# Kernel tuning notes

Measured on AMD Instinct MI355X. Metric: run time of the kernel, lower is better.

Reference implementation:

```python
import jax, jax.numpy as jnp
import numpy as np

B, S, H = 4, 2048, 1024
NH = 16
HD = H // NH  # 64


def setup_inputs() -> dict:
    key = jax.random.key(0)
    ks = jax.random.split(key, 9)
    s = 1.0 / np.sqrt(H)
    inp = {
        "x": jax.random.normal(ks[0], (B, S, H), dtype=jnp.float32),
        "wq": jax.random.normal(ks[1], (H, H), dtype=jnp.float32) * s,
        "bq": jnp.zeros((H,), dtype=jnp.float32),
        "wk": jax.random.normal(ks[2], (H, H), dtype=jnp.float32) * s,
        "bk": jnp.zeros((H,), dtype=jnp.float32),
        "wv": jax.random.normal(ks[3], (H, H), dtype=jnp.float32) * s,
        "bv": jnp.zeros((H,), dtype=jnp.float32),
        "wo": jax.random.normal(ks[4], (H, H), dtype=jnp.float32) * s,
        "bo": jnp.zeros((H,), dtype=jnp.float32),
    }
    return inp


def _split_heads(t):
    # [B,S,H] -> [B,NH,S,HD]
    return t.reshape(B, S, NH, HD).transpose(0, 2, 1, 3)


def reference(x, wq, bq, wk, bk, wv, bv, wo, bo):
    # Linear layers (torch Linear: x @ W^T + b; weights here stored as [in,out])
    q = _split_heads(x @ wq + bq)
    k = _split_heads(x @ wk + bk)
    v = _split_heads(x @ wv + bv)
    scale = 1.0 / jnp.sqrt(jnp.asarray(HD, dtype=x.dtype))
    scores = jnp.einsum("bhqd,bhkd->bhqk", q, k) * scale  # [B,NH,S,S]
    attn = jax.nn.softmax(scores, axis=-1)
    ctx = jnp.einsum("bhqk,bhkd->bhqd", attn, v)  # [B,NH,S,HD]
    ctx = ctx.transpose(0, 2, 1, 3).reshape(B, S, H)
    return ctx @ wo + bo
```

## Files before the change

kernel.cpp:

```cpp
#include <hip/hip_runtime.h>
#include <hip/hip_bf16.h>
#include <math.h>

typedef __bf16 bf16;
typedef __attribute__((ext_vector_type(4))) __bf16 bf16x4;
typedef __attribute__((ext_vector_type(8))) __bf16 bf16x8;
typedef __attribute__((ext_vector_type(4))) float f32x4;

#define B_  4
#define S_  2048
#define H_  1024
#define NH_ 16
#define HD_ 64
#define M_  (B_ * S_)

#define LP 72

__device__ __forceinline__ f32x4 mfma16(bf16x8 a, bf16x8 b, f32x4 c) {
    return __builtin_amdgcn_mfma_f32_16x16x32_bf16(a, b, c, 0, 0, 0);
}

__device__ __forceinline__ void glds16(const bf16* g, bf16* l) {
    __builtin_amdgcn_global_load_lds(
        (const __attribute__((address_space(1))) void*)g,
        (__attribute__((address_space(3))) void*)l, 16, 0, 0);
}

__global__ __launch_bounds__(256) void cvt_bf16(const float* __restrict__ in,
                                                bf16* __restrict__ out) {
    const size_t i = ((size_t)blockIdx.x * 256 + threadIdx.x) * 8;
    float4 f0 = *(const float4*)&in[i];
    float4 f1 = *(const float4*)&in[i + 4];
    bf16x8 v;
    v[0] = (bf16)f0.x; v[1] = (bf16)f0.y; v[2] = (bf16)f0.z; v[3] = (bf16)f0.w;
    v[4] = (bf16)f1.x; v[5] = (bf16)f1.y; v[6] = (bf16)f1.z; v[7] = (bf16)f1.w;
    *(bf16x8*)&out[i] = v;
}

__global__ __launch_bounds__(256) void transpose_w(const float* __restrict__ in,
                                                   bf16* __restrict__ out) {
    __shared__ bf16 tile[64][65];
    const int t = threadIdx.x;
    const int bx = blockIdx.x * 64, by = blockIdx.y * 64;
#pragma unroll
    for (int i = 0; i < 16; ++i) {
        int idx = i * 256 + t;
        int r = idx >> 6, c = idx & 63;
        tile[r][c] = (bf16)in[(by + r) * 1024 + bx + c];
    }
    __syncthreads();
#pragma unroll
    for (int i = 0; i < 16; ++i) {
        int idx = i * 256 + t;
        int r = idx >> 6, c = idx & 63;
        out[(bx + r) * 1024 + by + c] = tile[c][r];
    }
}

template <typename TC0>
__global__ __launch_bounds__(256) void gemm_glds(const bf16* __restrict__ A,
                                                 const bf16* __restrict__ Bt,
                                                 const float* __restrict__ b0,
                                                 const float* __restrict__ b1,
                                                 const float* __restrict__ b2,
                                                 TC0* __restrict__ out0,
                                                 bf16* __restrict__ out1,
                                                 bf16* __restrict__ out2t,
                                                 float scale0) {
    __shared__ alignas(16) bf16 As[128 * 64];
    __shared__ alignas(16) bf16 Bs[128 * 64];
    const int t = threadIdx.x;
    const int m0 = blockIdx.x * 128;
    const int n0 = blockIdx.y * 128;
    const int lane = t & 63, w = t >> 6;
    const int quad = lane >> 4, l15 = lane & 15;
    const int wm = w >> 1, wn = w & 1;
    const int srow = lane >> 3;
    const int scol = (lane & 7) * 8;

    const bf16* Ab = A + (size_t)(m0 + srow) * 1024 + scol;
    const bf16* Bb = Bt + (size_t)(n0 + srow) * 1024 + scol;

    f32x4 acc[4][4];
#pragma unroll
    for (int i = 0; i < 4; ++i)
#pragma unroll
        for (int j = 0; j < 4; ++j) acc[i][j] = (f32x4){0.f, 0.f, 0.f, 0.f};

    for (int kt = 0; kt < 16; ++kt) {
#pragma unroll
        for (int i = 0; i < 4; ++i) {
            const int c = w * 4 + i;
            glds16(Ab + (size_t)c * 8 * 1024 + kt * 64, &As[c * 512]);
            glds16(Bb + (size_t)c * 8 * 1024 + kt * 64, &Bs[c * 512]);
        }
        __syncthreads();
#pragma unroll
        for (int ks = 0; ks < 2; ++ks) {
            bf16x8 a[4], b[4];
#pragma unroll
            for (int mi = 0; mi < 4; ++mi)
                a[mi] = *(const bf16x8*)&As[(wm * 64 + mi * 16 + l15) * 64 + ks * 32 + quad * 8];
#pragma unroll
            for (int ni = 0; ni < 4; ++ni)
                b[ni] = *(const bf16x8*)&Bs[(wn * 64 + ni * 16 + l15) * 64 + ks * 32 + quad * 8];
#pragma unroll
            for (int mi = 0; mi < 4; ++mi)
#pragma unroll
                for (int ni = 0; ni < 4; ++ni)
                    acc[mi][ni] = mfma16(a[mi], b[ni], acc[mi][ni]);
        }
        __syncthreads();
    }

    const int seg = n0 >> 10;
    const float* bias = (seg == 0) ? b0 : (seg == 1) ? b1 : b2;
#pragma unroll
    for (int ni = 0; ni < 4; ++ni) {
        const int coln = (n0 & 1023) + wn * 64 + ni * 16 + l15;
        const float bcol = bias[coln];
#pragma unroll
        for (int mi = 0; mi < 4; ++mi) {
            const int row0 = m0 + wm * 64 + mi * 16 + quad * 4;
            if (seg == 2) {
                bf16x4 v;
#pragma unroll
                for (int r = 0; r < 4; ++r) v[r] = (bf16)(acc[mi][ni][r] + bcol);
                *(bf16x4*)&out2t[(size_t)coln * M_ + row0] = v;
            } else if (seg == 1) {
#pragma unroll
                for (int r = 0; r < 4; ++r)
                    out1[(size_t)(row0 + r) * 1024 + coln] = (bf16)(acc[mi][ni][r] + bcol);
            } else {
#pragma unroll
                for (int r = 0; r < 4; ++r)
                    out0[(size_t)(row0 + r) * 1024 + coln] =
                        (TC0)((acc[mi][ni][r] + bcol) * scale0);
            }
        }
    }
}

__global__ __launch_bounds__(256, 4) void attn(const bf16* Q,
                                               const bf16* __restrict__ K,
                                               const bf16* __restrict__ Vt,
                                               bf16* O) {
    __shared__ alignas(16) bf16 smem[128 * LP];
    bf16* Ks = smem;
    bf16* Vs = smem + 64 * LP;

    const int t = threadIdx.x;
    const int lane = t & 63, w = t >> 6;
    const int quad = lane >> 4, l15 = lane & 15;
    const int bh = blockIdx.x;
    const int q0 = blockIdx.y * 128;
    const int b = bh >> 4, h = bh & 15;
    const bf16* qp  = Q + (size_t)b * S_ * H_ + h * HD_;
    const bf16* kp  = K + (size_t)b * S_ * H_ + h * HD_;
    const bf16* vtp = Vt + (size_t)(h * HD_) * M_ + b * S_;

    const int r0 = t >> 3, r1 = 32 + (t >> 3);
    const int kc = (t & 7) * 8;
    const int s0 = ((((r0 >> 4) & 2) | ((r0 >> 2) & 1)) << 4) + (((r0 >> 3) & 3) << 2) + (r0 & 3);
    const int s1 = ((((r1 >> 4) & 2) | ((r1 >> 2) & 1)) << 4) + (((r1 >> 3) & 3) << 2) + (r1 & 3);

    bf16x8 kpre[2], vpre[2];
    kpre[0] = *(const bf16x8*)&kp[(size_t)r0 * H_ + kc];
    kpre[1] = *(const bf16x8*)&kp[(size_t)r1 * H_ + kc];
    vpre[0] = *(const bf16x8*)&vtp[(size_t)r0 * M_ + kc];
    vpre[1] = *(const bf16x8*)&vtp[(size_t)r1 * M_ + kc];

#pragma unroll
    for (int i = 0; i < 4; ++i) {
        int c = i * 256 + t;
        int row = c >> 3, qkc = (c & 7) * 8;
        *(bf16x8*)&smem[row * LP + qkc] =
            *(const bf16x8*)&qp[(size_t)(q0 + row) * H_ + qkc];
    }
    __syncthreads();
    bf16x8 aq[2][2];
#pragma unroll
    for (int mi = 0; mi < 2; ++mi)
#pragma unroll
        for (int ks = 0; ks < 2; ++ks)
            aq[mi][ks] = *(const bf16x8*)
                &smem[(w * 32 + mi * 16 + l15) * LP + ks * 32 + quad * 8];

    bf16x8 ones;
#pragma unroll
    for (int j = 0; j < 8; ++j) ones[j] = (bf16)1.0f;

    f32x4 o[2][4];
    f32x4 lsum[2];
#pragma unroll
    for (int mi = 0; mi < 2; ++mi) {
        lsum[mi] = (f32x4){0.f, 0.f, 0.f, 0.f};
#pragma unroll
        for (int i = 0; i < 4; ++i) o[mi][i] = (f32x4){0.f, 0.f, 0.f, 0.f};
    }

    for (int kt = 0; kt < S_ / 64; ++kt) {
        __syncthreads();
        *(bf16x8*)&Ks[s0 * LP + kc] = kpre[0];
        *(bf16x8*)&Ks[s1 * LP + kc] = kpre[1];
        *(bf16x8*)&Vs[r0 * LP + kc] = vpre[0];
        *(bf16x8*)&Vs[r1 * LP + kc] = vpre[1];
        __syncthreads();

        if (kt + 1 < S_ / 64) {
            const int key1 = (kt + 1) * 64;
            kpre[0] = *(const bf16x8*)&kp[(size_t)(key1 + r0) * H_ + kc];
            kpre[1] = *(const bf16x8*)&kp[(size_t)(key1 + r1) * H_ + kc];
            vpre[0] = *(const bf16x8*)&vtp[(size_t)r0 * M_ + key1 + kc];
            vpre[1] = *(const bf16x8*)&vtp[(size_t)r1 * M_ + key1 + kc];
        }

        f32x4 scT[2][4];
#pragma unroll
        for (int kb = 0; kb < 4; ++kb) {
            bf16x8 k0 = *(const bf16x8*)&Ks[(kb * 16 + l15) * LP + quad * 8];
            bf16x8 k1 = *(const bf16x8*)&Ks[(kb * 16 + l15) * LP + 32 + quad * 8];
#pragma unroll
            for (int mi = 0; mi < 2; ++mi) {
                scT[mi][kb] = mfma16(k0, aq[mi][0], (f32x4){0.f, 0.f, 0.f, 0.f});
                scT[mi][kb] = mfma16(k1, aq[mi][1], scT[mi][kb]);
            }
        }

        bf16x8 ap[2][2];
#pragma unroll
        for (int mi = 0; mi < 2; ++mi)
#pragma unroll
            for (int ks = 0; ks < 2; ++ks) {
                bf16x8 v;
#pragma unroll
                for (int j = 0; j < 4; ++j) v[j] = (bf16)__expf(scT[mi][2 * ks][j]);
#pragma unroll
                for (int j = 0; j < 4; ++j) v[4 + j] = (bf16)__expf(scT[mi][2 * ks + 1][j]);
                ap[mi][ks] = v;
            }

#pragma unroll
        for (int ks = 0; ks < 2; ++ks) {
#pragma unroll
            for (int mi = 0; mi < 2; ++mi)
                lsum[mi] = mfma16(ap[mi][ks], ones, lsum[mi]);
#pragma unroll
            for (int dt = 0; dt < 4; ++dt) {
                bf16x8 bv = *(const bf16x8*)&Vs[(dt * 16 + l15) * LP + ks * 32 + quad * 8];
#pragma unroll
                for (int mi = 0; mi < 2; ++mi)
                    o[mi][dt] = mfma16(ap[mi][ks], bv, o[mi][dt]);
            }
        }
    }

#pragma unroll
    for (int mi = 0; mi < 2; ++mi)
#pragma unroll
        for (int r = 0; r < 4; ++r) {
            float inv = 1.f / lsum[mi][r];
            int row = q0 + w * 32 + mi * 16 + quad * 4 + r;
            size_t base = (size_t)b * S_ * H_ + (size_t)row * H_ + h * HD_;
#pragma unroll
            for (int dt = 0; dt < 4; ++dt)
                O[base + dt * 16 + l15] = (bf16)(o[mi][dt][r] * inv);
        }
}

extern "C" void kernel_launch(void* const* d_in, const int* in_sizes, int n_in,
                              void* d_out, int out_size, void* d_ws, size_t ws_size,
                              hipStream_t stream) {
    const float* x  = (const float*)d_in[0];
    const float* wq = (const float*)d_in[1];
    const float* bq = (const float*)d_in[2];
    const float* wk = (const float*)d_in[3];
    const float* bk = (const float*)d_in[4];
    const float* wv = (const float*)d_in[5];
    const float* bv = (const float*)d_in[6];
    const float* wo = (const float*)d_in[7];
    const float* bo = (const float*)d_in[8];

    bf16* ws = (bf16*)d_ws;
    const size_t WSZ = 1024 * 1024;
    const size_t TSZ = (size_t)M_ * H_;
    bf16* wt  = ws;
    bf16* qb  = wt + WSZ;
    bf16* kb  = qb + TSZ;
    bf16* vbt = kb + TSZ;
    bf16* ctx = qb;

    bf16* xb    = (bf16*)d_out;
    bf16* wqkvt = xb + TSZ;

    cvt_bf16<<<dim3(M_ * H_ / (256 * 8)), 256, 0, stream>>>(x, xb);

    dim3 tgrid(16, 16);
    transpose_w<<<tgrid, 256, 0, stream>>>(wq, wqkvt);
    transpose_w<<<tgrid, 256, 0, stream>>>(wk, wqkvt + WSZ);
    transpose_w<<<tgrid, 256, 0, stream>>>(wv, wqkvt + 2 * WSZ);

    dim3 qkvgrid(M_ / 128, 3072 / 128);
    gemm_glds<bf16><<<qkvgrid, 256, 0, stream>>>(xb, wqkvt, bq, bk, bv,
                                                 qb, kb, vbt, 0.125f);

    dim3 agrid(B_ * NH_, S_ / 128);
    attn<<<agrid, 256, 0, stream>>>(qb, kb, vbt, ctx);

    transpose_w<<<tgrid, 256, 0, stream>>>(wo, wt);
    dim3 ogrid(M_ / 128, 1024 / 128);
    gemm_glds<float><<<ogrid, 256, 0, stream>>>(ctx, wt, bo, bo, bo,
                                                (float*)d_out, nullptr, nullptr, 1.0f);
}
```

Before: 280.1 us.

## Add 256x256-tile 8-wave QKV GEMM with phased double-buffered LDS pipeline

Replaces the 128x128 QKV projection GEMM with a dedicated kernel that uses 256x256 output tiles, 512 threads (8 waves), and a double-buffered LDS pipeline split into half-K phases. Global-to-LDS loads for the next stage are interleaved with MFMA clusters, using explicit waitcnt, barriers and setprio. The block index is swizzled to improve L2 reuse. Each operand tile is reused across more output, which cuts global/LDS traffic per FLOP, at the cost of higher register pressure and a grid of only 384 blocks. The generic GEMM is simplified for the output projection only.

```diff
diff --git a/kernel.cpp b/kernel.cpp
--- a/kernel.cpp
+++ b/kernel.cpp
@@ -57,15 +57,150 @@
     }
 }
 
+__global__ __launch_bounds__(512, 2) void gemm_qkv_8ph(const bf16* __restrict__ A,
+                                                       const bf16* __restrict__ Bt,
+                                                       const float* __restrict__ b0,
+                                                       const float* __restrict__ b1,
+                                                       const float* __restrict__ b2,
+                                                       bf16* __restrict__ out0,
+                                                       bf16* __restrict__ out1,
+                                                       bf16* __restrict__ out2t,
+                                                       float scale0) {
+    __shared__ alignas(16) bf16 As[2 * 2 * 256 * 32];
+    __shared__ alignas(16) bf16 Bs[2 * 2 * 256 * 32];
+    const int td = threadIdx.x;
+    const int lane = td & 63, w = td >> 6;
+    const int quad = lane >> 4, l15 = lane & 15;
+    const int wm = w >> 2, wn = w & 3;
+
+    const int bid = blockIdx.x;
+    const int lin = (bid & 7) * 48 + (bid >> 3);
+    const int m0 = (lin & 31) * 256;
+    const int n0 = (lin >> 5) * 256;
+
+    const int srow = td >> 2;
+    const int scol = (td & 3) * 8;
+    const bf16* Ag = A + (size_t)(m0 + srow) * 1024 + scol;
+    const bf16* Bg = Bt + (size_t)(n0 + srow) * 1024 + scol;
+
+    auto stageA = [&](int buf, int h, int kt) {
+        const bf16* g = Ag + kt * 64 + h * 32;
+        bf16* l = &As[(buf * 2 + h) * 8192 + w * 512];
+        glds16(g, l);
+        glds16(g + 128 * 1024, l + 4096);
+        __builtin_amdgcn_sched_barrier(0);
+    };
+    auto stageB = [&](int buf, int h, int kt) {
+        const bf16* g = Bg + kt * 64 + h * 32;
+        bf16* l = &Bs[(buf * 2 + h) * 8192 + w * 512];
+        glds16(g, l);
+        glds16(g + 128 * 1024, l + 4096);
+        __builtin_amdgcn_sched_barrier(0);
+    };
+
+    f32x4 acc[8][4];
+#pragma unroll
+    for (int i = 0; i < 8; ++i)
+#pragma unroll
+        for (int j = 0; j < 4; ++j) acc[i][j] = (f32x4){0.f, 0.f, 0.f, 0.f};
+
+#define LDS_A(buf, s, mi) (*(const bf16x8*)&As[((buf) * 2 + (s)) * 8192 + \
+        (wm * 128 + (mi) * 16 + l15) * 32 + quad * 8])
+#define LDS_B(buf, s, nj) (*(const bf16x8*)&Bs[((buf) * 2 + (s)) * 8192 + \
+        (wn * 64 + (nj) * 16 + l15) * 32 + quad * 8])
+#define MFMA_CL(QN)                                                   \
+    __builtin_amdgcn_s_setprio(1);                                    \
+    _Pragma("unroll")                                                 \
+    for (int mi = 0; mi < 8; ++mi) {                                  \
+        acc[mi][(QN) * 2]     = mfma16(af[mi], bf0, acc[mi][(QN) * 2]);     \
+        acc[mi][(QN) * 2 + 1] = mfma16(af[mi], bf1, acc[mi][(QN) * 2 + 1]); \
+    }                                                                 \
+    __builtin_amdgcn_s_setprio(0);
+
+    stageA(0, 0, 0); stageB(0, 0, 0); stageA(0, 1, 0); stageB(0, 1, 0);
+
+    bf16x8 af[8], bf0, bf1;
+#pragma unroll 1
+    for (int t = 0; t < 15; ++t) {
+        const int buf = t & 1, nbuf = buf ^ 1;
+        asm volatile("s_waitcnt vmcnt(4)" ::: "memory");
+        __builtin_amdgcn_s_barrier();
+        stageA(nbuf, 0, t + 1);
+#pragma unroll
+        for (int mi = 0; mi < 8; ++mi) af[mi] = LDS_A(buf, 0, mi);
+        bf0 = LDS_B(buf, 0, 0); bf1 = LDS_B(buf, 0, 1);
+        MFMA_CL(0)
+        __builtin_amdgcn_s_barrier();
+        stageB(nbuf, 0, t + 1);
+        bf0 = LDS_B(buf, 0, 2); bf1 = LDS_B(buf, 0, 3);
+        MFMA_CL(1)
+        asm volatile("s_waitcnt vmcnt(4)" ::: "memory");
+        __builtin_amdgcn_s_barrier();
+        stageA(nbuf, 1, t + 1);
+#pragma unroll
+        for (int mi = 0; mi < 8; ++mi) af[mi] = LDS_A(buf, 1, mi);
+        bf0 = LDS_B(buf, 1, 0); bf1 = LDS_B(buf, 1, 1);
+        MFMA_CL(0)
+        __builtin_amdgcn_s_barrier();
+        stageB(nbuf, 1, t + 1);
+        bf0 = LDS_B(buf, 1, 2); bf1 = LDS_B(buf, 1, 3);
+        MFMA_CL(1)
+    }
+    {
+        asm volatile("s_waitcnt vmcnt(4)" ::: "memory");
+        __builtin_amdgcn_s_barrier();
+#pragma unroll
+        for (int mi = 0; mi < 8; ++mi) af[mi] = LDS_A(1, 0, mi);
+        bf0 = LDS_B(1, 0, 0); bf1 = LDS_B(1, 0, 1);
+        MFMA_CL(0)
+        bf0 = LDS_B(1, 0, 2); bf1 = LDS_B(1, 0, 3);
+        MFMA_CL(1)
+        asm volatile("s_waitcnt vmcnt(0)" ::: "memory");
+        __builtin_amdgcn_s_barrier();
+#pragma unroll
+        for (int mi = 0; mi < 8; ++mi) af[mi] = LDS_A(1, 1, mi);
+        bf0 = LDS_B(1, 1, 0); bf1 = LDS_B(1, 1, 1);
+        MFMA_CL(0)
+        bf0 = LDS_B(1, 1, 2); bf1 = LDS_B(1, 1, 3);
+        MFMA_CL(1)
+    }
+#undef LDS_A
+#undef LDS_B
+#undef MFMA_CL
+
+    const int seg = n0 >> 10;
+    const float* bias = (seg == 0) ? b0 : (seg == 1) ? b1 : b2;
+#pragma unroll
+    for (int ni = 0; ni < 4; ++ni) {
+        const int coln = (n0 & 1023) + wn * 64 + ni * 16 + l15;
+        const float bcol = bias[coln];
+#pragma unroll
+        for (int mi = 0; mi < 8; ++mi) {
+            const int row0 = m0 + wm * 128 + mi * 16 + quad * 4;
+            if (seg == 2) {
+                bf16x4 v;
+#pragma unroll
+                for (int r = 0; r < 4; ++r) v[r] = (bf16)(acc[mi][ni][r] + bcol);
+                *(bf16x4*)&out2t[(size_t)coln * M_ + row0] = v;
+            } else if (seg == 1) {
+#pragma unroll
+                for (int r = 0; r < 4; ++r)
+                    out1[(size_t)(row0 + r) * 1024 + coln] = (bf16)(acc[mi][ni][r] + bcol);
+            } else {
+#pragma unroll
+                for (int r = 0; r < 4; ++r)
+                    out0[(size_t)(row0 + r) * 1024 + coln] =
+                        (bf16)((acc[mi][ni][r] + bcol) * scale0);
+            }
+        }
+    }
+}
+
 template <typename TC0>
 __global__ __launch_bounds__(256) void gemm_glds(const bf16* __restrict__ A,
                                                  const bf16* __restrict__ Bt,
                                                  const float* __restrict__ b0,
-                                                 const float* __restrict__ b1,
-                                                 const float* __restrict__ b2,
                                                  TC0* __restrict__ out0,
-                                                 bf16* __restrict__ out1,
-                                                 bf16* __restrict__ out2t,
                                                  float scale0) {
     __shared__ alignas(16) bf16 As[128 * 64];
     __shared__ alignas(16) bf16 Bs[128 * 64];
@@ -113,30 +248,17 @@
         __syncthreads();
     }
 
-    const int seg = n0 >> 10;
-    const float* bias = (seg == 0) ? b0 : (seg == 1) ? b1 : b2;
 #pragma unroll
     for (int ni = 0; ni < 4; ++ni) {
-        const int coln = (n0 & 1023) + wn * 64 + ni * 16 + l15;
-        const float bcol = bias[coln];
+        const int coln = n0 + wn * 64 + ni * 16 + l15;
+        const float bcol = b0[coln];
 #pragma unroll
         for (int mi = 0; mi < 4; ++mi) {
             const int row0 = m0 + wm * 64 + mi * 16 + quad * 4;
-            if (seg == 2) {
-                bf16x4 v;
-#pragma unroll
-                for (int r = 0; r < 4; ++r) v[r] = (bf16)(acc[mi][ni][r] + bcol);
-                *(bf16x4*)&out2t[(size_t)coln * M_ + row0] = v;
-            } else if (seg == 1) {
-#pragma unroll
-                for (int r = 0; r < 4; ++r)
-                    out1[(size_t)(row0 + r) * 1024 + coln] = (bf16)(acc[mi][ni][r] + bcol);
-            } else {
-#pragma unroll
-                for (int r = 0; r < 4; ++r)
-                    out0[(size_t)(row0 + r) * 1024 + coln] =
-                        (TC0)((acc[mi][ni][r] + bcol) * scale0);
-            }
+#pragma unroll
+            for (int r = 0; r < 4; ++r)
+                out0[(size_t)(row0 + r) * 1024 + coln] =
+                    (TC0)((acc[mi][ni][r] + bcol) * scale0);
         }
     }
 }
@@ -300,15 +422,13 @@
     transpose_w<<<tgrid, 256, 0, stream>>>(wk, wqkvt + WSZ);
     transpose_w<<<tgrid, 256, 0, stream>>>(wv, wqkvt + 2 * WSZ);
 
-    dim3 qkvgrid(M_ / 128, 3072 / 128);
-    gemm_glds<bf16><<<qkvgrid, 256, 0, stream>>>(xb, wqkvt, bq, bk, bv,
-                                                 qb, kb, vbt, 0.125f);
+    gemm_qkv_8ph<<<dim3(384), 512, 0, stream>>>(xb, wqkvt, bq, bk, bv,
+                                                qb, kb, vbt, 0.125f);
 
     dim3 agrid(B_ * NH_, S_ / 128);
     attn<<<agrid, 256, 0, stream>>>(qb, kb, vbt, ctx);
 
     transpose_w<<<tgrid, 256, 0, stream>>>(wo, wt);
     dim3 ogrid(M_ / 128, 1024 / 128);
-    gemm_glds<float><<<ogrid, 256, 0, stream>>>(ctx, wt, bo, bo, bo,
-                                                (float*)d_out, nullptr, nullptr, 1.0f);
-}
+    gemm_glds<float><<<ogrid, 256, 0, stream>>>(ctx, wt, bo, (float*)d_out, 1.0f);
+}
```

Measured after the change: 314.3 us. 1.12x slower.
